# Kernel optimization log

Hardware: AMD Instinct MI355X
Metric: run time of the kernel (lower is better)

The kernel has to match this reference:

```python
import jax, jax.numpy as jnp
import numpy as np


def setup_inputs() -> dict:
    key = jax.random.key(0)
    x = jax.random.normal(key, (8192, 4096), dtype=jnp.float32)
    return {"x": x, "k": 1}


def reference(x, k):
    # torch.linalg.svdvals returns singular values in descending order;
    # jnp.linalg.svd with compute_uv=False does the same.
    s = jnp.linalg.svd(x, compute_uv=False)  # [min(m, n)], descending
    return jnp.sum(s[:k] ** 2)
```

## Files before the change

kernel.cpp:

```cpp
#include <hip/hip_runtime.h>
#include <hip/hip_fp16.h>
#include <math.h>


#define NROWS 8192
#define NCOLS 4096
#define T_STEPS 16
#define NBLK 512
#define RPC 8
#define NCHUNK 2
#define SPIN_LIMIT 200000L

typedef float f32x4_t __attribute__((ext_vector_type(4)));
typedef float f32x2_t __attribute__((ext_vector_type(2)));

__device__ __forceinline__ unsigned ic_ld_u32(const unsigned* p) {
    unsigned v;
    asm volatile("global_load_dword %0, %1, off sc0 sc1\n\ts_waitcnt vmcnt(0)"
                 : "=v"(v) : "v"(p) : "memory");
    return v;
}
__device__ __forceinline__ float ic_ld_f32(const float* p) {
    float v;
    asm volatile("global_load_dword %0, %1, off sc0 sc1\n\ts_waitcnt vmcnt(0)"
                 : "=v"(v) : "v"(p) : "memory");
    return v;
}
__device__ __forceinline__ void ic_st_u32(unsigned* p, unsigned v) {
    asm volatile("global_store_dword %0, %1, off sc0 sc1"
                 :: "v"(p), "v"(v) : "memory");
}
__device__ __forceinline__ void ic_st_f32(float* p, float v) {
    asm volatile("global_store_dword %0, %1, off sc0 sc1"
                 :: "v"(p), "v"(v) : "memory");
}
__device__ __forceinline__ void ic_st2_f32(float2* p, float2 v) {
    f32x2_t x; x.x = v.x; x.y = v.y;
    asm volatile("global_store_dwordx2 %0, %1, off sc0 sc1"
                 :: "v"(p), "v"(x) : "memory");
}
__device__ __forceinline__ void ic_st4_f32(float* p, float4 v) {
    f32x4_t x; x.x = v.x; x.y = v.y; x.z = v.z; x.w = v.w;
    asm volatile("global_store_dwordx4 %0, %1, off sc0 sc1"
                 :: "v"(p), "v"(x) : "memory");
}
__device__ __forceinline__ unsigned ic_sum4_u32(const unsigned* p0, const unsigned* p1,
                                                const unsigned* p2, const unsigned* p3) {
    unsigned a, b, c, d;
    asm volatile(
        "global_load_dword %0, %4, off sc0 sc1\n\t"
        "global_load_dword %1, %5, off sc0 sc1\n\t"
        "global_load_dword %2, %6, off sc0 sc1\n\t"
        "global_load_dword %3, %7, off sc0 sc1\n\t"
        "s_waitcnt vmcnt(0)"
        : "=&v"(a), "=&v"(b), "=&v"(c), "=&v"(d)
        : "v"(p0), "v"(p1), "v"(p2), "v"(p3) : "memory");
    return a + b + c + d;
}
__device__ __forceinline__ void ic_ld4_f32x4(const float* p0, const float* p1,
                                             const float* p2, const float* p3,
                                             float4& ao, float4& bo, float4& co, float4& do_) {
    f32x4_t a, b, c, d;
    asm volatile(
        "global_load_dwordx4 %0, %4, off sc0 sc1\n\t"
        "global_load_dwordx4 %1, %5, off sc0 sc1\n\t"
        "global_load_dwordx4 %2, %6, off sc0 sc1\n\t"
        "global_load_dwordx4 %3, %7, off sc0 sc1\n\t"
        "s_waitcnt vmcnt(0)"
        : "=&v"(a), "=&v"(b), "=&v"(c), "=&v"(d)
        : "v"(p0), "v"(p1), "v"(p2), "v"(p3) : "memory");
    ao = make_float4(a.x, a.y, a.z, a.w);
    bo = make_float4(b.x, b.y, b.z, b.w);
    co = make_float4(c.x, c.y, c.z, c.w);
    do_ = make_float4(d.x, d.y, d.z, d.w);
}

__device__ __forceinline__ void up8(const float4& p, float* f) {
    const __half2* h = (const __half2*)&p;
    float2 t0 = __half22float2(h[0]);
    float2 t1 = __half22float2(h[1]);
    float2 t2 = __half22float2(h[2]);
    float2 t3 = __half22float2(h[3]);
    f[0] = t0.x; f[1] = t0.y; f[2] = t1.x; f[3] = t1.y;
    f[4] = t2.x; f[5] = t2.y; f[6] = t3.x; f[7] = t3.y;
}

__device__ __forceinline__ void gbar(unsigned* arrive, unsigned* release,
                                     unsigned* errw, unsigned gen, int bid) {
    __syncthreads();
    if (threadIdx.x == 0) {
        asm volatile("s_waitcnt vmcnt(0)" ::: "memory");
        __hip_atomic_fetch_add(&arrive[(bid & 7) * 16], 1u,
                               __ATOMIC_RELAXED, __HIP_MEMORY_SCOPE_AGENT);
        if (ic_ld_u32(errw) == 0) {
            long iters = 0;
            if (bid == 0) {
                const unsigned target = gen * NBLK;
                for (;;) {
                    unsigned s = ic_sum4_u32(&arrive[0], &arrive[16], &arrive[32], &arrive[48])
                               + ic_sum4_u32(&arrive[64], &arrive[80], &arrive[96], &arrive[112]);
                    if (s >= target) break;
                    if (++iters > SPIN_LIMIT) { ic_st_u32(errw, gen); break; }
                    if ((iters & 255) == 0 && ic_ld_u32(errw)) break;
                    __builtin_amdgcn_s_sleep(2);
                }
                ic_st_u32(release, gen);
            } else {
                while (ic_ld_u32(release) < gen) {
                    if (++iters > SPIN_LIMIT) { ic_st_u32(errw, gen); break; }
                    if ((iters & 255) == 0 && ic_ld_u32(errw)) break;
                    __builtin_amdgcn_s_sleep(2);
                }
            }
        }
    }
    __syncthreads();
}

__global__ __launch_bounds__(256, 4) void lanczos_fused(const float* __restrict__ A,
                                                        __half* __restrict__ Ah,
                                                        float* __restrict__ ws,
                                                        float* __restrict__ out) {
    __shared__ __align__(16) float smem[192];
    float* slots = ws + 12288;
    unsigned* arrive = (unsigned*)(ws + 12416);
    unsigned* release = (unsigned*)(ws + 12416) + 192;
    unsigned* errw = (unsigned*)(ws + 12416) + 200;
    float* partials = ws + 262144;
    const int tid = threadIdx.x;
    const int bid = blockIdx.x;
    const int gtid = bid * 256 + tid;
    unsigned gen = 0;

    {
        const float4* A4 = (const float4*)A;
        float2* O2 = (float2*)Ah;
#pragma unroll 4
        for (int i = gtid; i < (NROWS * NCOLS / 4); i += NBLK * 256) {
            float4 f = A4[i];
            union { float2 f2; __half2 h2[2]; } u;
            u.h2[0] = __halves2half2(__float2half_rn(f.x), __float2half_rn(f.y));
            u.h2[1] = __halves2half2(__float2half_rn(f.z), __float2half_rn(f.w));
            ic_st2_f32(O2 + i, u.f2);
        }
        if (gtid < NCOLS) {
            unsigned h = (unsigned)gtid * 2654435761u;
            h ^= h >> 16; h *= 2246822519u; h ^= h >> 13;
            ic_st_f32(ws + 4096 + gtid, (h & 1u) ? 0.015625f : -0.015625f);
            ic_st_f32(ws + gtid, 0.f);
            if (gtid < 128)
                ic_st_f32(slots + gtid, (gtid == 64 || gtid == 65) ? 1.f : 0.f);
        }
    }
    gbar(arrive, release, errw, ++gen, bid);

    for (int j = 1; j <= T_STEPS; ++j) {
        const float* rc = ws + 4096 * (j % 3);
        const float* rp = ws + 4096 * ((j + 2) % 3);
        float* wt = ws + 4096 * ((j + 1) % 3);

        {
            int lane = tid & 63;
            float inv = rsqrtf(fmaxf(ic_ld_f32(&slots[64 + j]), 1e-30f));
            int cA = tid * 8, cB = 2048 + tid * 8;
            float vA[8], vB[8];
            {
                float4 x, y, z, w4;
                ic_ld4_f32x4(rc + cA, rc + cA + 4, rc + cB, rc + cB + 4, x, y, z, w4);
                vA[0] = x.x * inv; vA[1] = x.y * inv; vA[2] = x.z * inv; vA[3] = x.w * inv;
                vA[4] = y.x * inv; vA[5] = y.y * inv; vA[6] = y.z * inv; vA[7] = y.w * inv;
                vB[0] = z.x * inv; vB[1] = z.y * inv; vB[2] = z.z * inv; vB[3] = z.w * inv;
                vB[4] = w4.x * inv; vB[5] = w4.y * inv; vB[6] = w4.z * inv; vB[7] = w4.w * inv;
            }
            float wacc[16];
#pragma unroll
            for (int i = 0; i < 16; ++i) wacc[i] = 0.f;
            float aa_tot = 0.f;

#pragma unroll 1
            for (int ch = 0; ch < NCHUNK; ++ch) {
                int row0 = ch * (NBLK * RPC) + bid * RPC;
                const __half* base = Ah + (size_t)row0 * NCOLS;
                float4 alo[RPC], ahi[RPC];
#pragma unroll
                for (int r = 0; r < RPC; ++r) {
                    alo[r] = *(const float4*)(base + (size_t)r * NCOLS + cA);
                    ahi[r] = *(const float4*)(base + (size_t)r * NCOLS + cB);
                }
                __syncthreads();
                if (tid < RPC) smem[tid] = 0.f;
                __syncthreads();
#pragma unroll
                for (int r = 0; r < RPC; ++r) {
                    float f[8];
                    up8(alo[r], f);
                    float sp = f[0] * vA[0] + f[1] * vA[1] + f[2] * vA[2] + f[3] * vA[3]
                             + f[4] * vA[4] + f[5] * vA[5] + f[6] * vA[6] + f[7] * vA[7];
                    up8(ahi[r], f);
                    sp += f[0] * vB[0] + f[1] * vB[1] + f[2] * vB[2] + f[3] * vB[3]
                        + f[4] * vB[4] + f[5] * vB[5] + f[6] * vB[6] + f[7] * vB[7];
#pragma unroll
                    for (int off = 32; off > 0; off >>= 1) sp += __shfl_xor(sp, off);
                    if (lane == 0) atomicAdd(&smem[r], sp);
                }
                __syncthreads();
                if (tid == 0) {
#pragma unroll
                    for (int r = 0; r < RPC; ++r) aa_tot += smem[r] * smem[r];
                }
#pragma unroll
                for (int r = 0; r < RPC; ++r) {
                    float s = smem[r];
                    float f[8];
                    up8(alo[r], f);
                    wacc[0] += s * f[0]; wacc[1] += s * f[1]; wacc[2] += s * f[2]; wacc[3] += s * f[3];
                    wacc[4] += s * f[4]; wacc[5] += s * f[5]; wacc[6] += s * f[6]; wacc[7] += s * f[7];
                    up8(ahi[r], f);
                    wacc[8] += s * f[0]; wacc[9] += s * f[1]; wacc[10] += s * f[2]; wacc[11] += s * f[3];
                    wacc[12] += s * f[4]; wacc[13] += s * f[5]; wacc[14] += s * f[6]; wacc[15] += s * f[7];
                }
            }
            if (tid == 0) atomicAdd(&slots[j], aa_tot);
            float* pb = partials + (size_t)bid * NCOLS;
            ic_st4_f32(pb + cA,     make_float4(wacc[0], wacc[1], wacc[2], wacc[3]));
            ic_st4_f32(pb + cA + 4, make_float4(wacc[4], wacc[5], wacc[6], wacc[7]));
            ic_st4_f32(pb + cB,     make_float4(wacc[8], wacc[9], wacc[10], wacc[11]));
            ic_st4_f32(pb + cB + 4, make_float4(wacc[12], wacc[13], wacc[14], wacc[15]));
        }
        gbar(arrive, release, errw, ++gen, bid);

        if (j < T_STEPS) {
            {
                int q = tid & 1, p0 = tid >> 1;
                const float* pb0 = partials + (size_t)p0 * NCOLS + bid * 8 + q * 4;
                float4 v0, v1, v2, v3;
                ic_ld4_f32x4(pb0, pb0 + (size_t)128 * NCOLS,
                             pb0 + (size_t)256 * NCOLS, pb0 + (size_t)384 * NCOLS,
                             v0, v1, v2, v3);
                float4 s;
                s.x = v0.x + v1.x + v2.x + v3.x;
                s.y = v0.y + v1.y + v2.y + v3.y;
                s.z = v0.z + v1.z + v2.z + v3.z;
                s.w = v0.w + v1.w + v2.w + v3.w;
#pragma unroll
                for (int off = 2; off <= 32; off <<= 1) {
                    s.x += __shfl_xor(s.x, off);
                    s.y += __shfl_xor(s.y, off);
                    s.z += __shfl_xor(s.z, off);
                    s.w += __shfl_xor(s.w, off);
                }
                int lane = tid & 63, wv = tid >> 6;
                if (lane < 2) *(float4*)&smem[wv * 8 + lane * 4] = s;
                __syncthreads();
                if (tid < 8) {
                    int col = bid * 8 + tid;
                    float wsum = smem[tid] + smem[8 + tid] + smem[16 + tid] + smem[24 + tid];
                    float a = ic_ld_f32(&slots[j]);
                    float n2j = fmaxf(ic_ld_f32(&slots[64 + j]), 1e-30f);
                    float n2m = fmaxf(ic_ld_f32(&slots[64 + j - 1]), 1e-30f);
                    float invj = rsqrtf(n2j);
                    float cb = sqrtf(n2j / n2m);
                    float rn = wsum - a * invj * ic_ld_f32(&rc[col]) - cb * ic_ld_f32(&rp[col]);
                    ic_st_f32(&wt[col], rn);
                    float p = rn * rn;
                    p += __shfl_xor(p, 1);
                    p += __shfl_xor(p, 2);
                    p += __shfl_xor(p, 4);
                    if (tid == 0) atomicAdd(&slots[64 + j + 1], p);
                }
            }
            gbar(arrive, release, errw, ++gen, bid);
        }
    }

    if (bid == 0) {
        const int t = T_STEPS;
        float* d_s = smem;
        float* e2_s = smem + 64;
        if (tid < 64) {
            d_s[tid] = (tid < t) ? ic_ld_f32(&slots[1 + tid]) : 0.f;
            e2_s[tid] = (tid < t - 1) ? ic_ld_f32(&slots[64 + tid + 2]) : 0.f;
        }
        __syncthreads();
        if (tid < 64) {
            int lane = tid;
            float e_here = sqrtf(e2_s[lane]);
            float e_prev = (lane > 0) ? sqrtf(e2_s[lane - 1]) : 0.f;
            float d = d_s[lane];
            float gersh = (lane < t) ? d + e_here + e_prev : 0.f;
            float dmax = (lane < t) ? d : 0.f;
#pragma unroll
            for (int off = 32; off > 0; off >>= 1) {
                gersh = fmaxf(gersh, __shfl_xor(gersh, off));
                dmax = fmaxf(dmax, __shfl_xor(dmax, off));
            }
            float lo = dmax, hi = gersh + 1e-3f;
            for (int round = 0; round < 3; ++round) {
                float stepw = (hi - lo) * (1.f / 64.f);
                float x = lo + stepw * (lane + 1);
                double qv = 1.0;
                int cnt = 0;
                for (int i = 0; i < t; ++i) {
                    double qi = (double)d_s[i] - (double)x - ((i > 0) ? (double)e2_s[i - 1] / qv : 0.0);
                    if (fabs(qi) < 1e-300) qi = -1e-300;
                    cnt += (qi < 0.0);
                    qv = qi;
                }
                unsigned long long m = __ballot(cnt < t);
                if (m) {
                    int h = 63 - __clzll(m);
                    lo = lo + stepw * (h + 1);
                    hi = lo + stepw;
                } else {
                    hi = lo + stepw;
                }
            }
            if (tid == 0) {
                unsigned e = ic_ld_u32(errw);
                out[0] = e ? (-1.0e7f - (float)e) : 0.5f * (lo + hi);
            }
        }
    }
}

extern "C" void kernel_launch(void* const* d_in, const int* in_sizes, int n_in,
                              void* d_out, int out_size, void* d_ws, size_t ws_size,
                              hipStream_t stream) {
    const float* A = (const float*)d_in[0];
    float* out = (float*)d_out;
    float* ws = (float*)d_ws;
    __half* Ah = (__half*)((char*)d_ws + (size_t)16 * 1024 * 1024);

    hipMemsetAsync((char*)d_ws + (size_t)12416 * 4, 0, 1024, stream);

    lanczos_fused<<<NBLK, 256, 0, stream>>>(A, Ah, ws, out);
}
```

Baseline: 1.041 ms.

## Keep fp16 matrix slice resident in registers across Lanczos steps

Instead of converting A to fp16 into a global workspace and reloading each block's rows every Lanczos step, each block loads its 16 contiguous rows once, packs them to fp16, and keeps them in registers for all steps. This removes the per-iteration global read of the half-precision matrix (about 64 MB per step) and the initial fp16 store. In exchange it raises register pressure (launch bounds drop from 4 to 2 blocks per CU) and changes the row-to-block mapping. Extra syncthreads and a shifted smem region avoid conflicts between the row-dot scratch and the reduction buffer.

```diff
diff --git a/kernel.cpp b/kernel.cpp
--- a/kernel.cpp
+++ b/kernel.cpp
@@ -7,12 +7,10 @@
 #define NCOLS 4096
 #define T_STEPS 16
 #define NBLK 512
-#define RPC 8
-#define NCHUNK 2
+#define RPB 16
 #define SPIN_LIMIT 200000L
 
 typedef float f32x4_t __attribute__((ext_vector_type(4)));
-typedef float f32x2_t __attribute__((ext_vector_type(2)));
 
 __device__ __forceinline__ unsigned ic_ld_u32(const unsigned* p) {
     unsigned v;
@@ -33,11 +31,6 @@
 __device__ __forceinline__ void ic_st_f32(float* p, float v) {
     asm volatile("global_store_dword %0, %1, off sc0 sc1"
                  :: "v"(p), "v"(v) : "memory");
-}
-__device__ __forceinline__ void ic_st2_f32(float2* p, float2 v) {
-    f32x2_t x; x.x = v.x; x.y = v.y;
-    asm volatile("global_store_dwordx2 %0, %1, off sc0 sc1"
-                 :: "v"(p), "v"(x) : "memory");
 }
 __device__ __forceinline__ void ic_st4_f32(float* p, float4 v) {
     f32x4_t x; x.x = v.x; x.y = v.y; x.z = v.z; x.w = v.w;
@@ -83,6 +76,14 @@
     float2 t3 = __half22float2(h[3]);
     f[0] = t0.x; f[1] = t0.y; f[2] = t1.x; f[3] = t1.y;
     f[4] = t2.x; f[5] = t2.y; f[6] = t3.x; f[7] = t3.y;
+}
+__device__ __forceinline__ float4 pack8(const float4& a, const float4& b) {
+    union { float4 f4; __half2 h2[4]; } u;
+    u.h2[0] = __halves2half2(__float2half_rn(a.x), __float2half_rn(a.y));
+    u.h2[1] = __halves2half2(__float2half_rn(a.z), __float2half_rn(a.w));
+    u.h2[2] = __halves2half2(__float2half_rn(b.x), __float2half_rn(b.y));
+    u.h2[3] = __halves2half2(__float2half_rn(b.z), __float2half_rn(b.w));
+    return u.f4;
 }
 
 __device__ __forceinline__ void gbar(unsigned* arrive, unsigned* release,
@@ -117,8 +118,7 @@
     __syncthreads();
 }
 
-__global__ __launch_bounds__(256, 4) void lanczos_fused(const float* __restrict__ A,
-                                                        __half* __restrict__ Ah,
+__global__ __launch_bounds__(256, 2) void lanczos_fused(const float* __restrict__ A,
                                                         float* __restrict__ ws,
                                                         float* __restrict__ out) {
     __shared__ __align__(16) float smem[192];
@@ -130,18 +130,21 @@
     const int tid = threadIdx.x;
     const int bid = blockIdx.x;
     const int gtid = bid * 256 + tid;
+    const int cA = tid * 8, cB = 2048 + tid * 8;
     unsigned gen = 0;
 
+    float4 arA[RPB], arB[RPB];
     {
-        const float4* A4 = (const float4*)A;
-        float2* O2 = (float2*)Ah;
-#pragma unroll 4
-        for (int i = gtid; i < (NROWS * NCOLS / 4); i += NBLK * 256) {
-            float4 f = A4[i];
-            union { float2 f2; __half2 h2[2]; } u;
-            u.h2[0] = __halves2half2(__float2half_rn(f.x), __float2half_rn(f.y));
-            u.h2[1] = __halves2half2(__float2half_rn(f.z), __float2half_rn(f.w));
-            ic_st2_f32(O2 + i, u.f2);
+        const float* base = A + (size_t)bid * RPB * NCOLS;
+#pragma unroll
+        for (int r = 0; r < RPB; ++r) {
+            const float* rowp = base + (size_t)r * NCOLS;
+            float4 a0 = *(const float4*)(rowp + cA);
+            float4 a1 = *(const float4*)(rowp + cA + 4);
+            float4 b0 = *(const float4*)(rowp + cB);
+            float4 b1 = *(const float4*)(rowp + cB + 4);
+            arA[r] = pack8(a0, a1);
+            arB[r] = pack8(b0, b1);
         }
         if (gtid < NCOLS) {
             unsigned h = (unsigned)gtid * 2654435761u;
@@ -162,7 +165,6 @@
         {
             int lane = tid & 63;
             float inv = rsqrtf(fmaxf(ic_ld_f32(&slots[64 + j]), 1e-30f));
-            int cA = tid * 8, cB = 2048 + tid * 8;
             float vA[8], vB[8];
             {
                 float4 x, y, z, w4;
@@ -172,55 +174,43 @@
                 vB[0] = z.x * inv; vB[1] = z.y * inv; vB[2] = z.z * inv; vB[3] = z.w * inv;
                 vB[4] = w4.x * inv; vB[5] = w4.y * inv; vB[6] = w4.z * inv; vB[7] = w4.w * inv;
             }
+            __syncthreads();
+            if (tid < RPB) smem[tid] = 0.f;
+            __syncthreads();
+#pragma unroll
+            for (int r = 0; r < RPB; ++r) {
+                float f[8];
+                up8(arA[r], f);
+                float sp = f[0] * vA[0] + f[1] * vA[1] + f[2] * vA[2] + f[3] * vA[3]
+                         + f[4] * vA[4] + f[5] * vA[5] + f[6] * vA[6] + f[7] * vA[7];
+                up8(arB[r], f);
+                sp += f[0] * vB[0] + f[1] * vB[1] + f[2] * vB[2] + f[3] * vB[3]
+                    + f[4] * vB[4] + f[5] * vB[5] + f[6] * vB[6] + f[7] * vB[7];
+#pragma unroll
+                for (int off = 32; off > 0; off >>= 1) sp += __shfl_xor(sp, off);
+                if (lane == 0) atomicAdd(&smem[r], sp);
+            }
+            __syncthreads();
+            if (tid == 0) {
+                float aa = 0.f;
+#pragma unroll
+                for (int r = 0; r < RPB; ++r) aa += smem[r] * smem[r];
+                atomicAdd(&slots[j], aa);
+            }
             float wacc[16];
 #pragma unroll
             for (int i = 0; i < 16; ++i) wacc[i] = 0.f;
-            float aa_tot = 0.f;
-
-#pragma unroll 1
-            for (int ch = 0; ch < NCHUNK; ++ch) {
-                int row0 = ch * (NBLK * RPC) + bid * RPC;
-                const __half* base = Ah + (size_t)row0 * NCOLS;
-                float4 alo[RPC], ahi[RPC];
-#pragma unroll
-                for (int r = 0; r < RPC; ++r) {
-                    alo[r] = *(const float4*)(base + (size_t)r * NCOLS + cA);
-                    ahi[r] = *(const float4*)(base + (size_t)r * NCOLS + cB);
-                }
-                __syncthreads();
-                if (tid < RPC) smem[tid] = 0.f;
-                __syncthreads();
-#pragma unroll
-                for (int r = 0; r < RPC; ++r) {
-                    float f[8];
-                    up8(alo[r], f);
-                    float sp = f[0] * vA[0] + f[1] * vA[1] + f[2] * vA[2] + f[3] * vA[3]
-                             + f[4] * vA[4] + f[5] * vA[5] + f[6] * vA[6] + f[7] * vA[7];
-                    up8(ahi[r], f);
-                    sp += f[0] * vB[0] + f[1] * vB[1] + f[2] * vB[2] + f[3] * vB[3]
-                        + f[4] * vB[4] + f[5] * vB[5] + f[6] * vB[6] + f[7] * vB[7];
-#pragma unroll
-                    for (int off = 32; off > 0; off >>= 1) sp += __shfl_xor(sp, off);
-                    if (lane == 0) atomicAdd(&smem[r], sp);
-                }
-                __syncthreads();
-                if (tid == 0) {
-#pragma unroll
-                    for (int r = 0; r < RPC; ++r) aa_tot += smem[r] * smem[r];
-                }
-#pragma unroll
-                for (int r = 0; r < RPC; ++r) {
-                    float s = smem[r];
-                    float f[8];
-                    up8(alo[r], f);
-                    wacc[0] += s * f[0]; wacc[1] += s * f[1]; wacc[2] += s * f[2]; wacc[3] += s * f[3];
-                    wacc[4] += s * f[4]; wacc[5] += s * f[5]; wacc[6] += s * f[6]; wacc[7] += s * f[7];
-                    up8(ahi[r], f);
-                    wacc[8] += s * f[0]; wacc[9] += s * f[1]; wacc[10] += s * f[2]; wacc[11] += s * f[3];
-                    wacc[12] += s * f[4]; wacc[13] += s * f[5]; wacc[14] += s * f[6]; wacc[15] += s * f[7];
-                }
-            }
-            if (tid == 0) atomicAdd(&slots[j], aa_tot);
+#pragma unroll
+            for (int r = 0; r < RPB; ++r) {
+                float s = smem[r];
+                float f[8];
+                up8(arA[r], f);
+                wacc[0] += s * f[0]; wacc[1] += s * f[1]; wacc[2] += s * f[2]; wacc[3] += s * f[3];
+                wacc[4] += s * f[4]; wacc[5] += s * f[5]; wacc[6] += s * f[6]; wacc[7] += s * f[7];
+                up8(arB[r], f);
+                wacc[8] += s * f[0]; wacc[9] += s * f[1]; wacc[10] += s * f[2]; wacc[11] += s * f[3];
+                wacc[12] += s * f[4]; wacc[13] += s * f[5]; wacc[14] += s * f[6]; wacc[15] += s * f[7];
+            }
             float* pb = partials + (size_t)bid * NCOLS;
             ic_st4_f32(pb + cA,     make_float4(wacc[0], wacc[1], wacc[2], wacc[3]));
             ic_st4_f32(pb + cA + 4, make_float4(wacc[4], wacc[5], wacc[6], wacc[7]));
@@ -250,11 +240,12 @@
                     s.w += __shfl_xor(s.w, off);
                 }
                 int lane = tid & 63, wv = tid >> 6;
-                if (lane < 2) *(float4*)&smem[wv * 8 + lane * 4] = s;
+                __syncthreads();
+                if (lane < 2) *(float4*)&smem[32 + wv * 8 + lane * 4] = s;
                 __syncthreads();
                 if (tid < 8) {
                     int col = bid * 8 + tid;
-                    float wsum = smem[tid] + smem[8 + tid] + smem[16 + tid] + smem[24 + tid];
+                    float wsum = smem[32 + tid] + smem[40 + tid] + smem[48 + tid] + smem[56 + tid];
                     float a = ic_ld_f32(&slots[j]);
                     float n2j = fmaxf(ic_ld_f32(&slots[64 + j]), 1e-30f);
                     float n2m = fmaxf(ic_ld_f32(&slots[64 + j - 1]), 1e-30f);
@@ -329,9 +320,8 @@
     const float* A = (const float*)d_in[0];
     float* out = (float*)d_out;
     float* ws = (float*)d_ws;
-    __half* Ah = (__half*)((char*)d_ws + (size_t)16 * 1024 * 1024);
 
     hipMemsetAsync((char*)d_ws + (size_t)12416 * 4, 0, 1024, stream);
 
-    lanczos_fused<<<NBLK, 256, 0, stream>>>(A, Ah, ws, out);
-}
+    lanczos_fused<<<NBLK, 256, 0, stream>>>(A, ws, out);
+}
```

Measured after the change: 911.9 us. 1.14x faster.
